# Kernel tuning notes

Hardware: AMD Instinct MI355X
Metric: run time of the kernel (lower is better)

Reference implementation:

```python
import jax, jax.numpy as jnp
import numpy as np

N_HEADS = 8
EMBED = 640
CROSS = 768
HEAD = EMBED // N_HEADS


def setup_inputs() -> dict:
    key = jax.random.key(0)
    ks = jax.random.split(key, 10)
    s_e = 1.0 / np.sqrt(EMBED)
    s_c = 1.0 / np.sqrt(CROSS)
    return {
        "x": jax.random.normal(ks[0], (8, 4096, EMBED), jnp.float32),
        "y": jax.random.normal(ks[1], (8, 77, CROSS), jnp.float32),
        "Wq": jax.random.uniform(ks[2], (EMBED, EMBED), jnp.float32, -s_e, s_e),
        "bq": jax.random.uniform(ks[3], (EMBED,), jnp.float32, -s_e, s_e),
        "Wk": jax.random.uniform(ks[4], (CROSS, EMBED), jnp.float32, -s_c, s_c),
        "bk": jax.random.uniform(ks[5], (EMBED,), jnp.float32, -s_c, s_c),
        "Wv": jax.random.uniform(ks[6], (CROSS, EMBED), jnp.float32, -s_c, s_c),
        "bv": jax.random.uniform(ks[7], (EMBED,), jnp.float32, -s_c, s_c),
        "Wo": jax.random.uniform(ks[8], (EMBED, EMBED), jnp.float32, -s_e, s_e),
        "bo": jax.random.uniform(ks[9], (EMBED,), jnp.float32, -s_e, s_e),
    }


def reference(x, y, Wq, bq, Wk, bk, Wv, bv, Wo, bo):
    B, T, C = x.shape
    S = y.shape[1]
    # projections; split heads: [B, H, T, D]
    q = (x @ Wq + bq).reshape(B, T, N_HEADS, HEAD).transpose(0, 2, 1, 3)
    k = (y @ Wk + bk).reshape(B, S, N_HEADS, HEAD).transpose(0, 2, 1, 3)
    v = (y @ Wv + bv).reshape(B, S, N_HEADS, HEAD).transpose(0, 2, 1, 3)
    scores = jnp.einsum("bhtd,bhsd->bhts", q, k) / jnp.sqrt(jnp.float32(HEAD))
    attn = jax.nn.softmax(scores, axis=-1)
    out = jnp.einsum("bhts,bhsd->bhtd", attn, v)
    out = out.transpose(0, 2, 1, 3).reshape(B, T, C)
    return out @ Wo + bo
```

## Files before the change

kernel.cpp:

```cpp
#include <hip/hip_runtime.h>
#include <hip/hip_bf16.h>
#include <hip/hip_fp16.h>

#define EMBED 640
#define CROSS 768
#define NH 8
#define HEAD 80
#define BATCH 8
#define SEQT 4096
#define SEQS 77
#define MROWS (BATCH * SEQT)

typedef _Float16 half8 __attribute__((ext_vector_type(8)));
typedef float floatx4 __attribute__((ext_vector_type(4)));

__device__ __forceinline__ void lds_load16(const void* g, void* l) {
    __builtin_amdgcn_global_load_lds(
        (const __attribute__((address_space(1))) void*)g,
        (__attribute__((address_space(3))) void*)l, 16, 0, 0);
}

__global__ __launch_bounds__(256) void cvt_f32_f16(
    const float* __restrict__ in, _Float16* __restrict__ out)
{
    size_t i = ((size_t)blockIdx.x * 256 + threadIdx.x) * 8;
    float4 a = *(const float4*)&in[i];
    float4 b = *(const float4*)&in[i + 4];
    half8 h;
    h[0] = (_Float16)a.x; h[1] = (_Float16)a.y;
    h[2] = (_Float16)a.z; h[3] = (_Float16)a.w;
    h[4] = (_Float16)b.x; h[5] = (_Float16)b.y;
    h[6] = (_Float16)b.z; h[7] = (_Float16)b.w;
    *(half8*)&out[i] = h;
}

__global__ __launch_bounds__(256) void cvt_y_f16(
    const float* __restrict__ y, _Float16* __restrict__ yh)
{
    size_t i = ((size_t)blockIdx.x * 256 + threadIdx.x) * 8;
    half8 h = {};
    if (i < (size_t)BATCH * SEQS * CROSS) {
        float4 a = *(const float4*)&y[i];
        float4 b = *(const float4*)&y[i + 4];
        h[0] = (_Float16)a.x; h[1] = (_Float16)a.y;
        h[2] = (_Float16)a.z; h[3] = (_Float16)a.w;
        h[4] = (_Float16)b.x; h[5] = (_Float16)b.y;
        h[6] = (_Float16)b.z; h[7] = (_Float16)b.w;
    }
    *(half8*)&yh[i] = h;
}

__global__ __launch_bounds__(256) void zero_f16(_Float16* __restrict__ p, size_t n8)
{
    size_t i = (size_t)blockIdx.x * 256 + threadIdx.x;
    if (i < n8) *(half8*)&p[i * 8] = (half8){};
}

__global__ __launch_bounds__(256) void transpose_cvt(
    const float* __restrict__ W, _Float16* __restrict__ Wt, int K, int N)
{
    __shared__ float t[32][33];
    const int k0 = blockIdx.y * 32, n0 = blockIdx.x * 32;
    for (int r = threadIdx.y; r < 32; r += 8)
        t[r][threadIdx.x] = W[(size_t)(k0 + r) * N + n0 + threadIdx.x];
    __syncthreads();
    for (int r = threadIdx.y; r < 32; r += 8)
        Wt[(size_t)(n0 + r) * K + k0 + threadIdx.x] = (_Float16)t[threadIdx.x][r];
}

template <bool HALF_OUT>
__global__ __launch_bounds__(256) void gemm_f16(
    const _Float16* __restrict__ A,
    const _Float16* __restrict__ Bt,
    const float* __restrict__ bias,
    void* __restrict__ Cout, int M, int N, int K, float scale)
{
    __shared__ _Float16 As[128 * 32];
    __shared__ _Float16 Bs[128 * 32];

    const int tid  = threadIdx.x;
    const int wave = tid >> 6;
    const int lane = tid & 63;
    const int quad = lane >> 4;
    const int l16  = lane & 15;

    const int l   = blockIdx.y * gridDim.x + blockIdx.x;
    const int inner = l >> 3;
    const int p   = (l & 7) + 8 * (inner / gridDim.x);
    const int nt  = inner % gridDim.x;
    const int m0 = p * 128, n0 = nt * 128;
    const int wm = (wave >> 1) * 64, wn = (wave & 1) * 64;

    const int row = tid >> 2;
    const int kch = ((tid & 3) ^ ((row >> 1) & 3)) * 8;
    const int cq  = (quad ^ ((l16 >> 1) & 3)) * 8;

    floatx4 acc[4][4] = {};

    for (int k0 = 0; k0 < K; k0 += 32) {
        const _Float16* ga0 = &A [(size_t)(m0 + row)      * K + k0 + kch];
        const _Float16* ga1 = &A [(size_t)(m0 + 64 + row) * K + k0 + kch];
        const _Float16* gb0 = &Bt[(size_t)(n0 + row)      * K + k0 + kch];
        const _Float16* gb1 = &Bt[(size_t)(n0 + 64 + row) * K + k0 + kch];
        lds_load16(ga0, &As[wave * 512]);
        lds_load16(ga1, &As[2048 + wave * 512]);
        lds_load16(gb0, &Bs[wave * 512]);
        lds_load16(gb1, &Bs[2048 + wave * 512]);
        __syncthreads();

        half8 a[4], b[4];
        #pragma unroll
        for (int i = 0; i < 4; ++i)
            a[i] = *(const half8*)&As[(wm + i * 16 + l16) * 32 + cq];
        #pragma unroll
        for (int j = 0; j < 4; ++j)
            b[j] = *(const half8*)&Bs[(wn + j * 16 + l16) * 32 + cq];
        #pragma unroll
        for (int i = 0; i < 4; ++i)
            #pragma unroll
            for (int j = 0; j < 4; ++j)
                acc[i][j] = __builtin_amdgcn_mfma_f32_16x16x32_f16(
                    a[i], b[j], acc[i][j], 0, 0, 0);
        __syncthreads();
    }

    float bcol[4];
    #pragma unroll
    for (int j = 0; j < 4; ++j) bcol[j] = bias[n0 + wn + j * 16 + l16];
    #pragma unroll
    for (int i = 0; i < 4; ++i)
        #pragma unroll
        for (int r = 0; r < 4; ++r) {
            const int m = m0 + wm + i * 16 + quad * 4 + r;
            #pragma unroll
            for (int j = 0; j < 4; ++j) {
                float v = (acc[i][j][r] + bcol[j]) * scale;
                const size_t off = (size_t)m * N + n0 + wn + j * 16 + l16;
                if (HALF_OUT) ((_Float16*)Cout)[off] = (_Float16)v;
                else          ((float*)Cout)[off] = v;
            }
        }
}

__global__ __launch_bounds__(256) void kv_gemm(
    const _Float16* __restrict__ yh,
    const _Float16* __restrict__ Wkt, const _Float16* __restrict__ Wvt,
    const float* __restrict__ bk, const float* __restrict__ bv,
    _Float16* __restrict__ kh, _Float16* __restrict__ vth)
{
    __shared__ _Float16 As[64 * 32];
    __shared__ _Float16 Bs[64 * 32];

    const int tid = threadIdx.x;
    const int wave = tid >> 6, lane = tid & 63;
    const int quad = lane >> 4, l16 = lane & 15;
    const int m0 = blockIdx.y * 64, n0 = blockIdx.x * 64;
    const bool isV = blockIdx.z != 0;
    const _Float16* Bt = isV ? Wvt : Wkt;
    const float* bias  = isV ? bv : bk;

    const int row = tid >> 2;
    const int kch = (tid & 3) * 8;

    floatx4 acc[4] = {};

    for (int k0 = 0; k0 < CROSS; k0 += 32) {
        lds_load16(&yh[(size_t)(m0 + row) * CROSS + k0 + kch], &As[wave * 512]);
        lds_load16(&Bt[(size_t)(n0 + row) * CROSS + k0 + kch], &Bs[wave * 512]);
        __syncthreads();
        half8 b = *(const half8*)&Bs[(wave * 16 + l16) * 32 + quad * 8];
        #pragma unroll
        for (int i = 0; i < 4; ++i) {
            half8 a = *(const half8*)&As[(i * 16 + l16) * 32 + quad * 8];
            acc[i] = __builtin_amdgcn_mfma_f32_16x16x32_f16(a, b, acc[i], 0, 0, 0);
        }
        __syncthreads();
    }

    const int n = n0 + wave * 16 + l16;
    const int h = n / HEAD, d = n % HEAD;
    const float bb = bias[n];
    #pragma unroll
    for (int i = 0; i < 4; ++i)
        #pragma unroll
        for (int r = 0; r < 4; ++r) {
            const int m = m0 + i * 16 + quad * 4 + r;
            if (m >= BATCH * SEQS) continue;
            const int b_ = m / SEQS, s = m % SEQS;
            const int bh = b_ * NH + h;
            const float v = acc[i][r] + bb;
            if (isV) vth[(size_t)bh * (HEAD * 80) + d * 80 + s] = (_Float16)v;
            else     kh [(size_t)bh * (SEQS * HEAD) + s * HEAD + d] = (_Float16)v;
        }
}

__global__ __launch_bounds__(256, 4) void attn_mfma(
    const _Float16* __restrict__ qh,
    const _Float16* __restrict__ kh,
    const _Float16* __restrict__ vth,
    _Float16* __restrict__ oh)
{
    constexpr int LS = 88;
    __shared__ _Float16 lds[(80 + 80 + 64) * LS + 8];
    _Float16* Ks = lds;
    _Float16* Vt = lds + 80 * LS;
    _Float16* Ps = lds + 160 * LS;

    const int tid = threadIdx.x;
    const int wave = tid >> 6, lane = tid & 63;
    const int quad = lane >> 4, l16 = lane & 15;
    const int bh = blockIdx.y;
    const int b = bh >> 3, h = bh & 7;
    const size_t row0 = (size_t)b * SEQT + (size_t)blockIdx.x * 256;
    const half8 hz = {};

    const _Float16* qp = qh + (row0 + wave * 16 + l16) * EMBED + h * HEAD;

    half8 qa0 = *(const half8*)&qp[quad * 8];
    half8 qa1 = *(const half8*)&qp[32 + quad * 8];
    half8 qa2 = (quad < 2) ? *(const half8*)&qp[64 + quad * 8] : hz;

    for (int idx = tid; idx < 80 * 11; idx += 256) {
        const int s = idx / 11, c = idx % 11;
        half8 v = hz;
        if (s < SEQS && c < 10)
            v = *(const half8*)&kh[(size_t)bh * (SEQS * HEAD) + s * HEAD + c * 8];
        *(half8*)&Ks[s * LS + c * 8] = v;
    }
    for (int idx = tid; idx < 80 * 11; idx += 256) {
        const int d = idx / 11, c = idx % 11;
        half8 v = hz;
        if (c < 10)
            v = *(const half8*)&vth[(size_t)bh * (HEAD * 80) + d * 80 + c * 8];
        *(half8*)&Vt[d * LS + c * 8] = v;
    }
    __syncthreads();

    for (int t = 0; t < 4; ++t) {
        floatx4 accs[5] = {};
        #pragma unroll
        for (int st = 0; st < 5; ++st) {
            const _Float16* kr = &Ks[(st * 16 + l16) * LS];
            half8 b0 = *(const half8*)&kr[quad * 8];
            half8 b1 = *(const half8*)&kr[32 + quad * 8];
            half8 b2 = *(const half8*)&kr[64 + quad * 8];
            accs[st] = __builtin_amdgcn_mfma_f32_16x16x32_f16(qa0, b0, accs[st], 0, 0, 0);
            accs[st] = __builtin_amdgcn_mfma_f32_16x16x32_f16(qa1, b1, accs[st], 0, 0, 0);
            accs[st] = __builtin_amdgcn_mfma_f32_16x16x32_f16(qa2, b2, accs[st], 0, 0, 0);
        }
        if (l16 >= 13) {
            accs[4][0] = -1e30f; accs[4][1] = -1e30f;
            accs[4][2] = -1e30f; accs[4][3] = -1e30f;
        }

        float recip[4];
        #pragma unroll
        for (int r = 0; r < 4; ++r) {
            float m = accs[0][r];
            #pragma unroll
            for (int st = 1; st < 5; ++st) m = fmaxf(m, accs[st][r]);
            m = fmaxf(m, __shfl_xor(m, 1));
            m = fmaxf(m, __shfl_xor(m, 2));
            m = fmaxf(m, __shfl_xor(m, 4));
            m = fmaxf(m, __shfl_xor(m, 8));
            float l = 0.f;
            const int row = wave * 16 + quad * 4 + r;
            #pragma unroll
            for (int st = 0; st < 5; ++st) {
                float e = __expf(accs[st][r] - m);
                l += e;
                Ps[row * LS + st * 16 + l16] = (_Float16)e;
            }
            l += __shfl_xor(l, 1);
            l += __shfl_xor(l, 2);
            l += __shfl_xor(l, 4);
            l += __shfl_xor(l, 8);
            recip[r] = 1.0f / l;
        }
        __syncthreads();

        half8 qn0 = hz, qn1 = hz, qn2 = hz;
        if (t < 3) {
            const _Float16* qn = qp + (size_t)(t + 1) * 64 * EMBED;
            qn0 = *(const half8*)&qn[quad * 8];
            qn1 = *(const half8*)&qn[32 + quad * 8];
            if (quad < 2) qn2 = *(const half8*)&qn[64 + quad * 8];
        }

        const _Float16* pr = &Ps[(wave * 16 + l16) * LS];
        half8 pa0 = *(const half8*)&pr[quad * 8];
        half8 pa1 = *(const half8*)&pr[32 + quad * 8];
        half8 pa2 = (quad < 2) ? *(const half8*)&pr[64 + quad * 8] : hz;
        __syncthreads();

        floatx4 acco[5] = {};
        #pragma unroll
        for (int dt = 0; dt < 5; ++dt) {
            const _Float16* vr = &Vt[(dt * 16 + l16) * LS];
            half8 b0 = *(const half8*)&vr[quad * 8];
            half8 b1 = *(const half8*)&vr[32 + quad * 8];
            half8 b2 = *(const half8*)&vr[64 + quad * 8];
            acco[dt] = __builtin_amdgcn_mfma_f32_16x16x32_f16(pa0, b0, acco[dt], 0, 0, 0);
            acco[dt] = __builtin_amdgcn_mfma_f32_16x16x32_f16(pa1, b1, acco[dt], 0, 0, 0);
            acco[dt] = __builtin_amdgcn_mfma_f32_16x16x32_f16(pa2, b2, acco[dt], 0, 0, 0);
        }

        #pragma unroll
        for (int r = 0; r < 4; ++r) {
            const size_t grow = row0 + t * 64 + wave * 16 + quad * 4 + r;
            #pragma unroll
            for (int dt = 0; dt < 5; ++dt)
                oh[grow * EMBED + h * HEAD + dt * 16 + l16] =
                    (_Float16)(acco[dt][r] * recip[r]);
        }

        qa0 = qn0; qa1 = qn1; qa2 = qn2;
    }
}

extern "C" void kernel_launch(void* const* d_in, const int* in_sizes, int n_in,
                              void* d_out, int out_size, void* d_ws, size_t ws_size,
                              hipStream_t stream)
{
    const float* x  = (const float*)d_in[0];
    const float* y  = (const float*)d_in[1];
    const float* Wq = (const float*)d_in[2];
    const float* bq = (const float*)d_in[3];
    const float* Wk = (const float*)d_in[4];
    const float* bk = (const float*)d_in[5];
    const float* Wv = (const float*)d_in[6];
    const float* bv = (const float*)d_in[7];
    const float* Wo = (const float*)d_in[8];
    const float* bo = (const float*)d_in[9];
    float* out = (float*)d_out;

    const size_t ME = (size_t)MROWS * EMBED;
    _Float16* xh  = (_Float16*)d_ws;
    _Float16* qh  = xh + ME;
    _Float16* ah  = qh + ME;
    _Float16* kh  = ah + ME;
    _Float16* vth = kh  + (size_t)BATCH * NH * SEQS * HEAD;
    _Float16* wqt = vth + (size_t)BATCH * NH * HEAD * 80;
    _Float16* wot = wqt + (size_t)EMBED * EMBED;
    _Float16* yh  = wot + (size_t)EMBED * EMBED;
    _Float16* wkt = yh  + (size_t)640 * CROSS;
    _Float16* wvt = wkt + (size_t)EMBED * CROSS;

    cvt_f32_f16<<<dim3(ME / (256 * 8)), 256, 0, stream>>>(x, xh);
    transpose_cvt<<<dim3(EMBED / 32, EMBED / 32), dim3(32, 8), 0, stream>>>(Wq, wqt, EMBED, EMBED);
    transpose_cvt<<<dim3(EMBED / 32, EMBED / 32), dim3(32, 8), 0, stream>>>(Wo, wot, EMBED, EMBED);
    transpose_cvt<<<dim3(EMBED / 32, CROSS / 32), dim3(32, 8), 0, stream>>>(Wk, wkt, CROSS, EMBED);
    transpose_cvt<<<dim3(EMBED / 32, CROSS / 32), dim3(32, 8), 0, stream>>>(Wv, wvt, CROSS, EMBED);
    cvt_y_f16<<<dim3(640 * CROSS / (256 * 8)), 256, 0, stream>>>(y, yh);
    zero_f16<<<dim3(((size_t)BATCH * NH * HEAD * 80 / 8 + 255) / 256), 256, 0, stream>>>(
        vth, (size_t)BATCH * NH * HEAD * 80 / 8);

    gemm_f16<true><<<dim3(EMBED / 128, MROWS / 128), 256, 0, stream>>>(
        xh, wqt, bq, qh, MROWS, EMBED, EMBED, 0.11180339887498949f);
    kv_gemm<<<dim3(EMBED / 64, 640 / 64, 2), 256, 0, stream>>>(
        yh, wkt, wvt, bk, bv, kh, vth);
    attn_mfma<<<dim3(SEQT / 256, BATCH * NH), 256, 0, stream>>>(qh, kh, vth, ah);
    gemm_f16<false><<<dim3(EMBED / 128, MROWS / 128), 256, 0, stream>>>(
        ah, wot, bo, out, MROWS, EMBED, EMBED, 1.0f);
}
```

Baseline: 306.6 us.

## Triple-buffer GEMM LDS tiles with async global-to-LDS prefetch

Replaces the single-buffered load-sync-compute loop in the f16 GEMM with a three-stage LDS ring. Global-to-LDS loads run up to three K-tiles ahead, and explicit vmcnt waits plus raw barriers take the place of __syncthreads. The aim is to hide global memory latency behind the MFMA work. In exchange LDS use per block triples to 48KB, which may cut occupancy, and correctness now rests on hand-written waitcnt counts.

```diff
diff --git a/kernel.cpp b/kernel.cpp
--- a/kernel.cpp
+++ b/kernel.cpp
@@ -75,8 +75,8 @@
     const float* __restrict__ bias,
     void* __restrict__ Cout, int M, int N, int K, float scale)
 {
-    __shared__ _Float16 As[128 * 32];
-    __shared__ _Float16 Bs[128 * 32];
+    __shared__ _Float16 As[3][128 * 32];
+    __shared__ _Float16 Bs[3][128 * 32];
 
     const int tid  = threadIdx.x;
     const int wave = tid >> 6;
@@ -95,33 +95,51 @@
     const int kch = ((tid & 3) ^ ((row >> 1) & 3)) * 8;
     const int cq  = (quad ^ ((l16 >> 1) & 3)) * 8;
 
+    const _Float16* pa0 = &A [(size_t)(m0 + row)      * K + kch];
+    const _Float16* pa1 = &A [(size_t)(m0 + 64 + row) * K + kch];
+    const _Float16* pb0 = &Bt[(size_t)(n0 + row)      * K + kch];
+    const _Float16* pb1 = &Bt[(size_t)(n0 + 64 + row) * K + kch];
+
+    const int NT = K / 32;
+
+    auto stage = [&](int t) {
+        const int bf = t % 3;
+        const int off = t * 32;
+        lds_load16(pa0 + off, &As[bf][wave * 512]);
+        lds_load16(pa1 + off, &As[bf][2048 + wave * 512]);
+        lds_load16(pb0 + off, &Bs[bf][wave * 512]);
+        lds_load16(pb1 + off, &Bs[bf][2048 + wave * 512]);
+    };
+    stage(0); stage(1); stage(2);
+
     floatx4 acc[4][4] = {};
 
-    for (int k0 = 0; k0 < K; k0 += 32) {
-        const _Float16* ga0 = &A [(size_t)(m0 + row)      * K + k0 + kch];
-        const _Float16* ga1 = &A [(size_t)(m0 + 64 + row) * K + k0 + kch];
-        const _Float16* gb0 = &Bt[(size_t)(n0 + row)      * K + k0 + kch];
-        const _Float16* gb1 = &Bt[(size_t)(n0 + 64 + row) * K + k0 + kch];
-        lds_load16(ga0, &As[wave * 512]);
-        lds_load16(ga1, &As[2048 + wave * 512]);
-        lds_load16(gb0, &Bs[wave * 512]);
-        lds_load16(gb1, &Bs[2048 + wave * 512]);
-        __syncthreads();
-
+    for (int t = 0; t < NT; ++t) {
+        const int rem = NT - 1 - t;
+        if (rem >= 2)      asm volatile("s_waitcnt vmcnt(8)" ::: "memory");
+        else if (rem == 1) asm volatile("s_waitcnt vmcnt(4)" ::: "memory");
+        else               asm volatile("s_waitcnt vmcnt(0)" ::: "memory");
+        __builtin_amdgcn_s_barrier();
+
+        const _Float16* as = As[t % 3];
+        const _Float16* bs = Bs[t % 3];
         half8 a[4], b[4];
         #pragma unroll
         for (int i = 0; i < 4; ++i)
-            a[i] = *(const half8*)&As[(wm + i * 16 + l16) * 32 + cq];
+            a[i] = *(const half8*)&as[(wm + i * 16 + l16) * 32 + cq];
         #pragma unroll
         for (int j = 0; j < 4; ++j)
-            b[j] = *(const half8*)&Bs[(wn + j * 16 + l16) * 32 + cq];
+            b[j] = *(const half8*)&bs[(wn + j * 16 + l16) * 32 + cq];
         #pragma unroll
         for (int i = 0; i < 4; ++i)
             #pragma unroll
             for (int j = 0; j < 4; ++j)
                 acc[i][j] = __builtin_amdgcn_mfma_f32_16x16x32_f16(
                     a[i], b[j], acc[i][j], 0, 0, 0);
-        __syncthreads();
+
+        asm volatile("s_waitcnt lgkmcnt(0)" ::: "memory");
+        __builtin_amdgcn_s_barrier();
+        if (t + 3 < NT) stage(t + 3);
     }
 
     float bcol[4];
```

After: 301.2 us. Within noise of the previous version (-1.8%).
